# Kernel tuning notes

Hardware: AMD Instinct MI355X
Metric: run time of the kernel (lower is better)

The kernel has to match this reference:

```python
import jax, jax.numpy as jnp
import numpy as np

N_HEADS = 32
N_KV_HEADS = 8
HEAD_DIM = 64


def _apply_rope(x, cos, sin):
    # x: [b, s, h, d]; cos/sin: [s, d//2]; interleaved real/imag pairs
    xr = x[..., 0::2]
    xi = x[..., 1::2]
    c = cos[None, :, None, :]
    s = sin[None, :, None, :]
    out_r = xr * c - xi * s
    out_i = xr * s + xi * c
    return jnp.stack([out_r, out_i], axis=-1).reshape(x.shape)


def setup_inputs() -> dict:
    key = jax.random.key(0)
    ks = jax.random.split(key, 10)
    b, s, dim = 2, 512, 2048
    cache_len = 1536
    half = HEAD_DIM // 2
    pos = jnp.arange(cache_len, cache_len + s, dtype=jnp.float32)
    inv_freq = 1.0 / (10000.0 ** (jnp.arange(0, half, dtype=jnp.float32) / half))
    ang = pos[:, None] * inv_freq[None, :]
    scale = 0.02
    return {
        "x": jax.random.normal(ks[0], (b, s, dim), jnp.float32),
        "freqs_cos": jnp.cos(ang),
        "freqs_sin": jnp.sin(ang),
        "k_cache": jax.random.normal(ks[1], (b, N_KV_HEADS, cache_len, HEAD_DIM), jnp.float32),
        "v_cache": jax.random.normal(ks[2], (b, N_KV_HEADS, cache_len, HEAD_DIM), jnp.float32),
        "attn_mask": jnp.zeros((s, cache_len + s), jnp.float32),
        "wq": jax.random.normal(ks[3], (N_HEADS * HEAD_DIM, dim), jnp.float32) * scale,
        "wk": jax.random.normal(ks[4], (N_KV_HEADS * HEAD_DIM, dim), jnp.float32) * scale,
        "wv": jax.random.normal(ks[5], (N_KV_HEADS * HEAD_DIM, dim), jnp.float32) * scale,
        "wo": jax.random.normal(ks[6], (dim, N_HEADS * HEAD_DIM), jnp.float32) * scale,
    }


def reference(x, freqs_cos, freqs_sin, k_cache, v_cache, attn_mask, wq, wk, wv, wo):
    b, s, dim = x.shape
    n_rep = N_HEADS // N_KV_HEADS
    # QKV projections (nn.Linear: y = x @ W.T)
    q = (x @ wq.T).reshape(b, s, N_HEADS, HEAD_DIM)
    k = (x @ wk.T).reshape(b, s, N_KV_HEADS, HEAD_DIM)
    v = (x @ wv.T).reshape(b, s, N_KV_HEADS, HEAD_DIM)
    # RoPE on q, k
    q = _apply_rope(q, freqs_cos, freqs_sin)
    k = _apply_rope(k, freqs_cos, freqs_sin)
    # [b, h, s, d]
    q = q.transpose(0, 2, 1, 3)
    k = k.transpose(0, 2, 1, 3)
    v = v.transpose(0, 2, 1, 3)
    new_k, new_v = k, v
    # KV-cache concat along sequence dim
    k_full = jnp.concatenate([k_cache, k], axis=2)
    v_full = jnp.concatenate([v_cache, v], axis=2)
    # GQA: repeat_interleave kv heads
    if n_rep > 1:
        k_full = jnp.repeat(k_full, n_rep, axis=1)
        v_full = jnp.repeat(v_full, n_rep, axis=1)
    # SDPA
    scale = 1.0 / jnp.sqrt(jnp.asarray(HEAD_DIM, x.dtype))
    scores = jnp.einsum("bhqd,bhkd->bhqk", q, k_full) * scale + attn_mask
    probs = jax.nn.softmax(scores, axis=-1)
    out = jnp.einsum("bhqk,bhkd->bhqd", probs, v_full)
    out = out.transpose(0, 2, 1, 3).reshape(b, s, N_HEADS * HEAD_DIM)
    out = out @ wo.T
    return (out, new_k, new_v)
```

## Files before the change

kernel.cpp:

```cpp
#include <hip/hip_runtime.h>
#include <hip/hip_bf16.h>

typedef __attribute__((ext_vector_type(8))) short bf16x8;
typedef __attribute__((ext_vector_type(4))) float f32x4;
typedef unsigned short u16;

#define MFMA16(a, b, c) __builtin_amdgcn_mfma_f32_16x16x32_bf16(a, b, c, 0, 0, 0)
#define GLL(srcp, dstp) __builtin_amdgcn_global_load_lds(                      \
    (const __attribute__((address_space(1))) void*)(srcp),                     \
    (__attribute__((address_space(3))) void*)(dstp), 16, 0, 0)

__device__ __forceinline__ u16 f2b(float f) {
  union { float f; unsigned u; } a; a.f = f;
  return (u16)((a.u + 0x7FFFu + ((a.u >> 16) & 1u)) >> 16);
}
__device__ __forceinline__ unsigned pk2(float lo, float hi) {
  __hip_bfloat162 h = __float22bfloat162_rn(make_float2(lo, hi));
  return *reinterpret_cast<unsigned*>(&h);
}

__global__ __launch_bounds__(256) void prep(const float* __restrict__ x,
                                            const float* __restrict__ kc,
                                            u16* __restrict__ xb,
                                            u16* __restrict__ kfull) {
  const int c = blockIdx.x * 256 + threadIdx.x;
  const float* src;
  u16* dst;
  if (c < 524288) {
    src = x + (size_t)c * 4; dst = xb + (size_t)c * 4;
  } else {
    int l = c - 524288;
    int bh = l / 24576, r = l - bh * 24576;
    src = kc + (size_t)bh * 98304 + (size_t)r * 4;
    dst = kfull + (size_t)bh * 131072 + (size_t)r * 4;
  }
  const float4 v = *(const float4*)src;
  ushort4 o;
  o.x = f2b(v.x); o.y = f2b(v.y); o.z = f2b(v.z); o.w = f2b(v.w);
  *(ushort4*)dst = o;
}

__global__ __launch_bounds__(256) void vtr(const float* __restrict__ vc,
                                           const float* __restrict__ newv,
                                           u16* __restrict__ vT) {
  __shared__ float tile[64][65];
  const int kt = blockIdx.x, bh = blockIdx.y;
  const float* src;
  int colbase;
  if (kt < 24) {
    src = vc + ((size_t)bh * 1536 + (size_t)kt * 64) * 64;
    colbase = kt * 64;
  } else {
    src = newv + ((size_t)bh * 512 + (size_t)(kt - 24) * 64) * 64;
    colbase = 1536 + (kt - 24) * 64;
  }
  const int t = threadIdx.x;
#pragma unroll
  for (int j = 0; j < 4; j++) {
    int e = t + j * 256;
    int r = e >> 4, c = (e & 15) * 4;
    float4 v = *(const float4*)(src + (size_t)r * 64 + c);
    tile[r][c] = v.x; tile[r][c + 1] = v.y; tile[r][c + 2] = v.z; tile[r][c + 3] = v.w;
  }
  __syncthreads();
  int d = t >> 2, kv0 = (t & 3) * 16;
  u16* dst = vT + ((size_t)bh * 64 + d) * 2048 + colbase + (kv0 >> 4);
#pragma unroll
  for (int i = 0; i < 16; i++) dst[i * 4] = f2b(tile[kv0 + i][d]);
}

__global__ __launch_bounds__(256, 3) void gemm_bt(const u16* __restrict__ A,
                                                  const float* __restrict__ B0,
                                                  const float* __restrict__ B1,
                                                  const float* __restrict__ B2,
                                                  float* __restrict__ Cp,
                                                  int M, int N, int K, int nb1, int nb2) {
  __shared__ __attribute__((aligned(16))) u16 As[2][4096];
  __shared__ __attribute__((aligned(16))) u16 Bs[2][8192];
  const int t = threadIdx.x;
  const int lane = t & 63, w = t >> 6;
  const int wr = (w >> 1) * 32, wc = (w & 1) * 64;
  const int g = lane >> 4, cc = lane & 15;
  const int nby = N >> 7, cpx = nby >> 3, nrt = M >> 6;
  const int j = blockIdx.x & 7, q = blockIdx.x >> 3;
  const int ct = j * cpx + (q % cpx);
  const int rest = q / cpx;
  const int rt = rest % nrt, ks = rest / nrt;
  const size_t row0 = (size_t)rt * 64;
  const int col0 = ct * 128;
  const int k0base = ks * (K >> 1);

  const int lr = lane >> 3, lc = lane & 7;
  const int swz = lc ^ lr;
  const u16* aS = A + (row0 + w * 16 + lr) * (size_t)K + swz * 8 + k0base;
  const float* Bb;
  int brow;
  if (col0 < nb1) { Bb = B0; brow = col0; }
  else if (col0 < nb2) { Bb = B1; brow = col0 - nb1; }
  else { Bb = B2; brow = col0 - nb2; }
  const float* bS = Bb + (brow + w * 32 + lr) * (size_t)K + swz * 8 + k0base;

  f32x4 acc[2][4] = {};
  f32x4 blA[4][2], blB[4][2];

#define ALOAD(bufi, kk0)                                                       \
  {                                                                            \
    _Pragma("unroll") for (int i = 0; i < 2; i++)                              \
        GLL(aS + (size_t)(i * 8) * K + (kk0), &As[bufi][(w * 16 + i * 8) * 64]); \
  }
#define BLOAD(blv, kk0)                                                        \
  {                                                                            \
    _Pragma("unroll") for (int i = 0; i < 4; i++) {                            \
      blv[i][0] = *(const f32x4*)(bS + (size_t)(i * 8) * K + (kk0));           \
      blv[i][1] = *(const f32x4*)(bS + (size_t)(i * 8) * K + (kk0) + 4);       \
    }                                                                          \
  }
#define BWRITE(blv, bufi)                                                      \
  {                                                                            \
    _Pragma("unroll") for (int i = 0; i < 4; i++) {                            \
      uint4 pw;                                                                \
      pw.x = pk2(blv[i][0][0], blv[i][0][1]);                                  \
      pw.y = pk2(blv[i][0][2], blv[i][0][3]);                                  \
      pw.z = pk2(blv[i][1][0], blv[i][1][1]);                                  \
      pw.w = pk2(blv[i][1][2], blv[i][1][3]);                                  \
      *(uint4*)&Bs[bufi][(w * 32 + i * 8 + lr) * 64 + lc * 8] = pw;            \
    }                                                                          \
  }

  const int niter = (K >> 1) >> 6;

  ALOAD(0, 0);
  BLOAD(blA, 0);
  BWRITE(blA, 0);
  BLOAD(blB, 64);
  asm volatile("s_waitcnt lgkmcnt(0)" ::: "memory");
  __builtin_amdgcn_s_barrier();

#define GBODY(it_, blPrev, blCur)                                              \
  {                                                                            \
    const int buf = (it_) & 1;                                                 \
    if ((it_) > 0) {                                                           \
      if ((it_) + 1 < niter) {                                                 \
        asm volatile("s_waitcnt vmcnt(8)" ::: "memory");                       \
      } else {                                                                 \
        asm volatile("s_waitcnt vmcnt(0)" ::: "memory");                       \
      }                                                                        \
      asm volatile("s_waitcnt lgkmcnt(0)" ::: "memory");                       \
      __builtin_amdgcn_s_barrier();                                            \
    }                                                                          \
    if ((it_) + 1 < niter) ALOAD(buf ^ 1, ((it_) + 1) * 64);                   \
    if ((it_) + 2 < niter) BLOAD(blCur, ((it_) + 2) * 64);                     \
    bf16x8 av[2][2], bv[4][2];                                                 \
    _Pragma("unroll") for (int m = 0; m < 2; m++) {                            \
      const int row = wr + m * 16 + cc;                                        \
      _Pragma("unroll") for (int kk = 0; kk < 2; kk++)                         \
          av[m][kk] =                                                          \
              *(const bf16x8*)(&As[buf][row * 64 + (((kk * 4 + g) ^ (cc & 7)) * 8)]); \
    }                                                                          \
    _Pragma("unroll") for (int n = 0; n < 4; n++) {                            \
      const int row = wc + n * 16 + cc;                                        \
      _Pragma("unroll") for (int kk = 0; kk < 2; kk++)                         \
          bv[n][kk] =                                                          \
              *(const bf16x8*)(&Bs[buf][row * 64 + (((kk * 4 + g) ^ (cc & 7)) * 8)]); \
    }                                                                          \
    _Pragma("unroll") for (int kk = 0; kk < 2; kk++)                           \
        _Pragma("unroll") for (int m = 0; m < 2; m++)                          \
        _Pragma("unroll") for (int n = 0; n < 4; n++)                          \
            acc[m][n] = MFMA16(av[m][kk], bv[n][kk], acc[m][n]);               \
    if ((it_) + 1 < niter) BWRITE(blPrev, buf ^ 1);                            \
  }

  for (int it = 0; it < niter; it += 2) {
    GBODY(it, blB, blA);
    GBODY(it + 1, blA, blB);
  }
#undef GBODY
#undef ALOAD
#undef BLOAD
#undef BWRITE

  float* Cw = Cp + (size_t)ks * M * N;
#pragma unroll
  for (int m = 0; m < 2; m++)
#pragma unroll
    for (int n = 0; n < 4; n++)
#pragma unroll
      for (int r = 0; r < 4; r++)
        Cw[(row0 + wr + m * 16 + g * 4 + r) * N + (col0 + wc + n * 16 + cc)] = acc[m][n][r];
}

__global__ __launch_bounds__(256) void postproc(const float* __restrict__ Cp0,
                                                const float* __restrict__ Cp1,
                                                const float* __restrict__ fcos,
                                                const float* __restrict__ fsin,
                                                u16* __restrict__ qrope,
                                                u16* __restrict__ kfull,
                                                float* __restrict__ newk,
                                                float* __restrict__ newv) {
  int idx = blockIdx.x * 256 + threadIdx.x;
  if (idx >= 1024 * 1536) return;
  int m = idx / 1536, p = idx - m * 1536;
  int b = m >> 9, s = m & 511;
  const float* r0 = Cp0 + (size_t)m * 3072;
  const float* r1 = Cp1 + (size_t)m * 3072;
  if (p < 1280) {
    bool isq = p < 1024;
    int pk = isq ? p : p - 1024;
    int h = pk >> 5, i = pk & 31;
    int colbase = (isq ? 0 : 2048) + h * 64 + 2 * i;
    float xr = r0[colbase] + r1[colbase];
    float xi = r0[colbase + 1] + r1[colbase + 1];
    float co = fcos[s * 32 + i], si = fsin[s * 32 + i];
    float orr = xr * co - xi * si;
    float oii = xr * si + xi * co;
    if (isq) {
      u16* dst = qrope + (((size_t)(b * 32 + h) * 512 + s) * 64 + 2 * i);
      dst[0] = f2b(orr); dst[1] = f2b(oii);
    } else {
      size_t o0 = ((size_t)(b * 8 + h) * 512 + s) * 64 + 2 * i;
      newk[o0] = orr; newk[o0 + 1] = oii;
      u16* kf = kfull + (((size_t)(b * 8 + h) * 2048 + 1536 + s) * 64 + 2 * i);
      kf[0] = f2b(orr); kf[1] = f2b(oii);
    }
  } else {
    int pv = p - 1280;
    int h = pv >> 5, i = pv & 31;
    int cb = 2560 + h * 64 + 2 * i;
    float v0 = r0[cb] + r1[cb], v1 = r0[cb + 1] + r1[cb + 1];
    size_t o0 = ((size_t)(b * 8 + h) * 512 + s) * 64 + 2 * i;
    newv[o0] = v0; newv[o0 + 1] = v1;
  }
}

__global__ __launch_bounds__(256) void sumout(const float* __restrict__ a,
                                              const float* __restrict__ b,
                                              float* __restrict__ out) {
  const int i = blockIdx.x * 256 + threadIdx.x;
  const float4 va = *(const float4*)(a + (size_t)i * 4);
  const float4 vb = *(const float4*)(b + (size_t)i * 4);
  float4 o;
  o.x = va.x + vb.x; o.y = va.y + vb.y; o.z = va.z + vb.z; o.w = va.w + vb.w;
  *(float4*)(out + (size_t)i * 4) = o;
}

__global__ __launch_bounds__(512, 4) void attn_split(const u16* __restrict__ qrope,
                                                     const u16* __restrict__ kfull,
                                                     const u16* __restrict__ vT,
                                                     const float* __restrict__ mask,
                                                     float* __restrict__ po,
                                                     float* __restrict__ ml) {
  __shared__ __attribute__((aligned(16))) u16 Ks[4][4096];
  __shared__ __attribute__((aligned(16))) u16 Vs[4][4096];
  __shared__ __attribute__((aligned(16))) u16 P_lds[8192];
  const int t = threadIdx.x, lane = t & 63, w = t >> 6;
  const int g = lane >> 4, cc = lane & 15;
  const int p = blockIdx.x;
  const int v = (p & 7) * 64 + (p >> 3);
  const int bh = v >> 3, qt = (v >> 1) & 3, sp = v & 1;
  const int b = bh >> 5, h = bh & 31;
  const int bhkv = b * 8 + (h >> 2);
  const int s0 = qt * 128 + w * 16;
  const int j0beg = sp * 1024;

  const int lr = lane >> 3, lc = lane & 7;
  const int swzc = lc ^ lr;

  bf16x8 qa0, qa1;
  {
    const u16* qb = qrope + ((size_t)bh * 512 + s0 + cc) * 64 + g * 8;
    qa0 = *(const bf16x8*)qb;
    qa1 = *(const bf16x8*)(qb + 32);
  }
  float mrow[4], lsum[4];
  f32x4 o[4] = {};
#pragma unroll
  for (int r = 0; r < 4; r++) { mrow[r] = -1e30f; lsum[r] = 0.0f; }

  u16* Pw = P_lds + w * 1024;
  const float* mbase = mask + (size_t)(s0 + g * 4) * 2048 + cc;
  const u16* ksrc0 = kfull + (size_t)bhkv * 131072 + (size_t)(w * 8 + lr) * 64 + swzc * 8;
  const u16* vsrc0 = vT + ((size_t)bhkv * 64 + w * 8 + lr) * 2048 + swzc * 8;

#pragma unroll
  for (int pt = 0; pt < 3; ++pt) {
    GLL(ksrc0 + (size_t)(j0beg + pt * 64) * 64, &Ks[pt][w * 512]);
    GLL(vsrc0 + (j0beg + pt * 64), &Vs[pt][w * 512]);
  }

  for (int it = 0; it < 16; ++it) {
    const int buf = it & 3;
    const int j0 = j0beg + it * 64;
    if (it < 14) {
      asm volatile("s_waitcnt vmcnt(4)" ::: "memory");
    } else if (it == 14) {
      asm volatile("s_waitcnt vmcnt(2)" ::: "memory");
    } else {
      asm volatile("s_waitcnt vmcnt(0)" ::: "memory");
    }
    __builtin_amdgcn_s_barrier();

    float mk[4][4];
#pragma unroll
    for (int r = 0; r < 4; r++)
#pragma unroll
      for (int jb = 0; jb < 4; jb++)
        mk[r][jb] = mbase[(size_t)r * 2048 + j0 + jb * 16];
    __builtin_amdgcn_sched_barrier(0);
    if (it < 13) {
      GLL(ksrc0 + (size_t)(j0 + 192) * 64, &Ks[(it + 3) & 3][w * 512]);
      GLL(vsrc0 + (j0 + 192), &Vs[(it + 3) & 3][w * 512]);
    }

    f32x4 sc[4];
    __builtin_amdgcn_s_setprio(1);
#pragma unroll
    for (int jb = 0; jb < 4; jb++) {
      const bf16x8 k0 = *(const bf16x8*)(&Ks[buf][(jb * 16 + cc) * 64 + ((g ^ (cc & 7)) * 8)]);
      const bf16x8 k1 =
          *(const bf16x8*)(&Ks[buf][(jb * 16 + cc) * 64 + (((g + 4) ^ (cc & 7)) * 8)]);
      f32x4 z = {0.f, 0.f, 0.f, 0.f};
      z = MFMA16(qa0, k0, z);
      z = MFMA16(qa1, k1, z);
      sc[jb] = z;
    }
    __builtin_amdgcn_s_setprio(0);
    float pp[4][4];
#pragma unroll
    for (int r = 0; r < 4; r++) {
#pragma unroll
      for (int jb = 0; jb < 4; jb++)
        pp[r][jb] = sc[jb][r] * 0.125f + mk[r][jb];
      const float lm = fmaxf(fmaxf(pp[r][0], pp[r][1]), fmaxf(pp[r][2], pp[r][3]));
      if (__any(lm > mrow[r] + 8.0f)) {
        float tm = lm;
#pragma unroll
        for (int off = 1; off < 16; off <<= 1) tm = fmaxf(tm, __shfl_xor(tm, off, 64));
        const float newm = fmaxf(mrow[r], tm);
        const float corr = __expf(mrow[r] - newm);
        mrow[r] = newm;
        lsum[r] *= corr;
#pragma unroll
        for (int db = 0; db < 4; db++) o[db][r] *= corr;
      }
      float ps = 0.f;
#pragma unroll
      for (int jb = 0; jb < 4; jb++) { pp[r][jb] = __expf(pp[r][jb] - mrow[r]); ps += pp[r][jb]; }
      lsum[r] += ps;
      const int rowb = (g * 4 + r) * 128;
      const int sw = ((g * 4 + r) & 7) << 4;
      uint2 pw;
      pw.x = pk2(pp[r][0], pp[r][1]);
      pw.y = pk2(pp[r][2], pp[r][3]);
      *(uint2*)((char*)Pw + ((rowb + cc * 8) ^ sw)) = pw;
    }
    __builtin_amdgcn_s_setprio(1);
#pragma unroll
    for (int kk = 0; kk < 2; kk++) {
      const bf16x8 pa =
          *(const bf16x8*)(Pw + (((cc * 128 + kk * 64 + g * 16) ^ ((cc & 7) << 4)) >> 1));
#pragma unroll
      for (int db = 0; db < 4; db++) {
        const bf16x8 vf =
            *(const bf16x8*)(&Vs[buf][(db * 16 + cc) * 64 + (((kk * 4 + g) ^ (cc & 7)) * 8)]);
        o[db] = MFMA16(pa, vf, o[db]);
      }
    }
    __builtin_amdgcn_s_setprio(0);
  }
#pragma unroll
  for (int r = 0; r < 4; r++) {
    float ps = lsum[r];
#pragma unroll
    for (int off = 1; off < 16; off <<= 1) ps += __shfl_xor(ps, off, 64);
    const size_t row = (size_t)bh * 512 + s0 + g * 4 + r;
    float* dst = po + (row * 2 + sp) * 64 + cc;
#pragma unroll
    for (int db = 0; db < 4; db++) dst[db * 16] = o[db][r];
    if (cc == 0) {
      float2* mlp = (float2*)ml;
      mlp[row * 2 + sp] = make_float2(mrow[r], ps);
    }
  }
}

__global__ __launch_bounds__(256) void attn_combine(const float* __restrict__ po,
                                                    const float* __restrict__ ml,
                                                    u16* __restrict__ aout) {
  const int t = threadIdx.x;
  const int row = blockIdx.x * 4 + (t >> 6);
  const int d = t & 63;
  const int bh = row >> 9, s = row & 511;
  const int b = bh >> 5, h = bh & 31;
  const float2* mlp = (const float2*)ml;
  const float2 m0 = mlp[row * 2 + 0], m1 = mlp[row * 2 + 1];
  const float M = fmaxf(m0.x, m1.x);
  const float w0 = __expf(m0.x - M), w1 = __expf(m1.x - M);
  const float L = m0.y * w0 + m1.y * w1;
  const float o = po[(size_t)(row * 2 + 0) * 64 + d] * w0 +
                  po[(size_t)(row * 2 + 1) * 64 + d] * w1;
  aout[((size_t)(b * 512 + s)) * 2048 + h * 64 + d] = f2b(o / L);
}

extern "C" void kernel_launch(void* const* d_in, const int* in_sizes, int n_in,
                              void* d_out, int out_size, void* d_ws, size_t ws_size,
                              hipStream_t stream) {
  (void)in_sizes; (void)n_in; (void)out_size; (void)ws_size;
  const float* x    = (const float*)d_in[0];
  const float* fcos = (const float*)d_in[1];
  const float* fsin = (const float*)d_in[2];
  const float* kc   = (const float*)d_in[3];
  const float* vc   = (const float*)d_in[4];
  const float* mask = (const float*)d_in[5];
  const float* wq   = (const float*)d_in[6];
  const float* wk   = (const float*)d_in[7];
  const float* wv   = (const float*)d_in[8];
  const float* wo   = (const float*)d_in[9];

  float* out_f = (float*)d_out;
  float* newk  = out_f + 2097152;
  float* newv  = out_f + 2621440;

  u16*   xb    = (u16*)d_ws;
  float* Cp    = (float*)(xb + 2097152);
  float* Cp1   = Cp + 3145728;
  u16*   qrope = (u16*)(Cp + 6291456);
  u16*   kfull = qrope + 2097152;
  u16*   vTf   = kfull + 2097152;
  u16*   aout  = vTf + 2097152;
  float* ml    = (float*)(aout + 2097152);
  float* po    = (float*)d_ws;
  float* Co    = (float*)d_ws;
  float* Co1   = Co + 2097152;

  prep<<<3584, 256, 0, stream>>>(x, kc, xb, kfull);

  gemm_bt<<<768, 256, 0, stream>>>(xb, wq, wk, wv, Cp,
                                   1024, 3072, 2048, 2048, 2560);
  postproc<<<6144, 256, 0, stream>>>(Cp, Cp1, fcos, fsin, qrope, kfull, newk, newv);
  vtr<<<dim3(32, 16), 256, 0, stream>>>(vc, newv, vTf);
  attn_split<<<512, 512, 0, stream>>>(qrope, kfull, vTf, mask, po, ml);
  attn_combine<<<8192, 256, 0, stream>>>(po, ml, aout);
  gemm_bt<<<512, 256, 0, stream>>>(aout, wo, wo, wo, Co,
                                   1024, 2048, 2048, 4096, 8192);
  sumout<<<2048, 256, 0, stream>>>(Co, Co1, out_f);
}
```

Measured before the change: 121.2 us.

## Split each attention block into two interleaved KV streams with independent softmax state

Each wave now runs two independent online-softmax accumulators over two halves of its KV range, which cuts the loop from 16 to 8 iterations, each handling two 64-key tiles. The QK MFMAs for the second stream are issued while the first stream's softmax and PV run, aiming to hide exp/shuffle latency behind matrix work. Prefetch changes from a 3-deep ring to double buffering with a full vmcnt(0) wait, which may expose more load latency. It also raises register pressure and adds a merge of the two partial results at the end.

```diff
diff --git a/kernel.cpp b/kernel.cpp
--- a/kernel.cpp
+++ b/kernel.cpp
@@ -271,89 +271,99 @@
     qa0 = *(const bf16x8*)qb;
     qa1 = *(const bf16x8*)(qb + 32);
   }
-  float mrow[4], lsum[4];
-  f32x4 o[4] = {};
-#pragma unroll
-  for (int r = 0; r < 4; r++) { mrow[r] = -1e30f; lsum[r] = 0.0f; }
+  float m0[4], l0[4], m1[4], l1[4];
+  f32x4 oa[4] = {}, ob[4] = {};
+#pragma unroll
+  for (int r = 0; r < 4; r++) { m0[r] = -1e30f; l0[r] = 0.f; m1[r] = -1e30f; l1[r] = 0.f; }
 
   u16* Pw = P_lds + w * 1024;
   const float* mbase = mask + (size_t)(s0 + g * 4) * 2048 + cc;
   const u16* ksrc0 = kfull + (size_t)bhkv * 131072 + (size_t)(w * 8 + lr) * 64 + swzc * 8;
   const u16* vsrc0 = vT + ((size_t)bhkv * 64 + w * 8 + lr) * 2048 + swzc * 8;
-
-#pragma unroll
-  for (int pt = 0; pt < 3; ++pt) {
-    GLL(ksrc0 + (size_t)(j0beg + pt * 64) * 64, &Ks[pt][w * 512]);
-    GLL(vsrc0 + (j0beg + pt * 64), &Vs[pt][w * 512]);
-  }
-
-  for (int it = 0; it < 16; ++it) {
-    const int buf = it & 3;
+  const u16* ksrc1 = ksrc0 + 512 * 64;
+  const u16* vsrc1 = vsrc0 + 512;
+
+  GLL(ksrc0 + (size_t)j0beg * 64, &Ks[0][w * 512]);
+  GLL(vsrc0 + j0beg, &Vs[0][w * 512]);
+  GLL(ksrc1 + (size_t)j0beg * 64, &Ks[2][w * 512]);
+  GLL(vsrc1 + j0beg, &Vs[2][w * 512]);
+
+  for (int it = 0; it < 8; ++it) {
+    const int bu = it & 1;
     const int j0 = j0beg + it * 64;
-    if (it < 14) {
-      asm volatile("s_waitcnt vmcnt(4)" ::: "memory");
-    } else if (it == 14) {
-      asm volatile("s_waitcnt vmcnt(2)" ::: "memory");
-    } else {
-      asm volatile("s_waitcnt vmcnt(0)" ::: "memory");
-    }
+    asm volatile("s_waitcnt vmcnt(0)" ::: "memory");
     __builtin_amdgcn_s_barrier();
 
-    float mk[4][4];
+    float mk0[4][4], mk1[4][4];
 #pragma unroll
     for (int r = 0; r < 4; r++)
 #pragma unroll
-      for (int jb = 0; jb < 4; jb++)
-        mk[r][jb] = mbase[(size_t)r * 2048 + j0 + jb * 16];
+      for (int jb = 0; jb < 4; jb++) {
+        mk0[r][jb] = mbase[(size_t)r * 2048 + j0 + jb * 16];
+        mk1[r][jb] = mbase[(size_t)r * 2048 + j0 + 512 + jb * 16];
+      }
     __builtin_amdgcn_sched_barrier(0);
-    if (it < 13) {
-      GLL(ksrc0 + (size_t)(j0 + 192) * 64, &Ks[(it + 3) & 3][w * 512]);
-      GLL(vsrc0 + (j0 + 192), &Vs[(it + 3) & 3][w * 512]);
-    }
-
-    f32x4 sc[4];
+    if (it < 7) {
+      GLL(ksrc0 + (size_t)(j0 + 64) * 64, &Ks[bu ^ 1][w * 512]);
+      GLL(vsrc0 + (j0 + 64), &Vs[bu ^ 1][w * 512]);
+      GLL(ksrc1 + (size_t)(j0 + 64) * 64, &Ks[2 + (bu ^ 1)][w * 512]);
+      GLL(vsrc1 + (j0 + 64), &Vs[2 + (bu ^ 1)][w * 512]);
+    }
+
+    f32x4 sc0[4];
     __builtin_amdgcn_s_setprio(1);
 #pragma unroll
     for (int jb = 0; jb < 4; jb++) {
-      const bf16x8 k0 = *(const bf16x8*)(&Ks[buf][(jb * 16 + cc) * 64 + ((g ^ (cc & 7)) * 8)]);
+      const bf16x8 k0 = *(const bf16x8*)(&Ks[bu][(jb * 16 + cc) * 64 + ((g ^ (cc & 7)) * 8)]);
       const bf16x8 k1 =
-          *(const bf16x8*)(&Ks[buf][(jb * 16 + cc) * 64 + (((g + 4) ^ (cc & 7)) * 8)]);
+          *(const bf16x8*)(&Ks[bu][(jb * 16 + cc) * 64 + (((g + 4) ^ (cc & 7)) * 8)]);
       f32x4 z = {0.f, 0.f, 0.f, 0.f};
       z = MFMA16(qa0, k0, z);
       z = MFMA16(qa1, k1, z);
-      sc[jb] = z;
+      sc0[jb] = z;
     }
     __builtin_amdgcn_s_setprio(0);
-    float pp[4][4];
 #pragma unroll
     for (int r = 0; r < 4; r++) {
-#pragma unroll
-      for (int jb = 0; jb < 4; jb++)
-        pp[r][jb] = sc[jb][r] * 0.125f + mk[r][jb];
-      const float lm = fmaxf(fmaxf(pp[r][0], pp[r][1]), fmaxf(pp[r][2], pp[r][3]));
-      if (__any(lm > mrow[r] + 8.0f)) {
+      float pp[4];
+#pragma unroll
+      for (int jb = 0; jb < 4; jb++) pp[jb] = sc0[jb][r] * 0.125f + mk0[r][jb];
+      const float lm = fmaxf(fmaxf(pp[0], pp[1]), fmaxf(pp[2], pp[3]));
+      if (__any(lm > m0[r] + 8.0f)) {
         float tm = lm;
 #pragma unroll
         for (int off = 1; off < 16; off <<= 1) tm = fmaxf(tm, __shfl_xor(tm, off, 64));
-        const float newm = fmaxf(mrow[r], tm);
-        const float corr = __expf(mrow[r] - newm);
-        mrow[r] = newm;
-        lsum[r] *= corr;
-#pragma unroll
-        for (int db = 0; db < 4; db++) o[db][r] *= corr;
+        const float newm = fmaxf(m0[r], tm);
+        const float corr = __expf(m0[r] - newm);
+        m0[r] = newm;
+        l0[r] *= corr;
+#pragma unroll
+        for (int db = 0; db < 4; db++) oa[db][r] *= corr;
       }
       float ps = 0.f;
 #pragma unroll
-      for (int jb = 0; jb < 4; jb++) { pp[r][jb] = __expf(pp[r][jb] - mrow[r]); ps += pp[r][jb]; }
-      lsum[r] += ps;
+      for (int jb = 0; jb < 4; jb++) { pp[jb] = __expf(pp[jb] - m0[r]); ps += pp[jb]; }
+      l0[r] += ps;
       const int rowb = (g * 4 + r) * 128;
       const int sw = ((g * 4 + r) & 7) << 4;
       uint2 pw;
-      pw.x = pk2(pp[r][0], pp[r][1]);
-      pw.y = pk2(pp[r][2], pp[r][3]);
+      pw.x = pk2(pp[0], pp[1]);
+      pw.y = pk2(pp[2], pp[3]);
       *(uint2*)((char*)Pw + ((rowb + cc * 8) ^ sw)) = pw;
     }
+    f32x4 sc1[4];
     __builtin_amdgcn_s_setprio(1);
+#pragma unroll
+    for (int jb = 0; jb < 4; jb++) {
+      const bf16x8 k0 =
+          *(const bf16x8*)(&Ks[2 + bu][(jb * 16 + cc) * 64 + ((g ^ (cc & 7)) * 8)]);
+      const bf16x8 k1 =
+          *(const bf16x8*)(&Ks[2 + bu][(jb * 16 + cc) * 64 + (((g + 4) ^ (cc & 7)) * 8)]);
+      f32x4 z = {0.f, 0.f, 0.f, 0.f};
+      z = MFMA16(qa0, k0, z);
+      z = MFMA16(qa1, k1, z);
+      sc1[jb] = z;
+    }
 #pragma unroll
     for (int kk = 0; kk < 2; kk++) {
       const bf16x8 pa =
@@ -361,24 +371,67 @@
 #pragma unroll
       for (int db = 0; db < 4; db++) {
         const bf16x8 vf =
-            *(const bf16x8*)(&Vs[buf][(db * 16 + cc) * 64 + (((kk * 4 + g) ^ (cc & 7)) * 8)]);
-        o[db] = MFMA16(pa, vf, o[db]);
+            *(const bf16x8*)(&Vs[bu][(db * 16 + cc) * 64 + (((kk * 4 + g) ^ (cc & 7)) * 8)]);
+        oa[db] = MFMA16(pa, vf, oa[db]);
       }
     }
     __builtin_amdgcn_s_setprio(0);
+#pragma unroll
+    for (int r = 0; r < 4; r++) {
+      float pp[4];
+#pragma unroll
+      for (int jb = 0; jb < 4; jb++) pp[jb] = sc1[jb][r] * 0.125f + mk1[r][jb];
+      const float lm = fmaxf(fmaxf(pp[0], pp[1]), fmaxf(pp[2], pp[3]));
+      if (__any(lm > m1[r] + 8.0f)) {
+        float tm = lm;
+#pragma unroll
+        for (int off = 1; off < 16; off <<= 1) tm = fmaxf(tm, __shfl_xor(tm, off, 64));
+        const float newm = fmaxf(m1[r], tm);
+        const float corr = __expf(m1[r] - newm);
+        m1[r] = newm;
+        l1[r] *= corr;
+#pragma unroll
+        for (int db = 0; db < 4; db++) ob[db][r] *= corr;
+      }
+      float ps = 0.f;
+#pragma unroll
+      for (int jb = 0; jb < 4; jb++) { pp[jb] = __expf(pp[jb] - m1[r]); ps += pp[jb]; }
+      l1[r] += ps;
+      const int rowb = (g * 4 + r) * 128;
+      const int sw = ((g * 4 + r) & 7) << 4;
+      uint2 pw;
+      pw.x = pk2(pp[0], pp[1]);
+      pw.y = pk2(pp[2], pp[3]);
+      *(uint2*)((char*)Pw + ((rowb + cc * 8) ^ sw)) = pw;
+    }
+    __builtin_amdgcn_s_setprio(1);
+#pragma unroll
+    for (int kk = 0; kk < 2; kk++) {
+      const bf16x8 pa =
+          *(const bf16x8*)(Pw + (((cc * 128 + kk * 64 + g * 16) ^ ((cc & 7) << 4)) >> 1));
+#pragma unroll
+      for (int db = 0; db < 4; db++) {
+        const bf16x8 vf =
+            *(const bf16x8*)(&Vs[2 + bu][(db * 16 + cc) * 64 + (((kk * 4 + g) ^ (cc & 7)) * 8)]);
+        ob[db] = MFMA16(pa, vf, ob[db]);
+      }
+    }
+    __builtin_amdgcn_s_setprio(0);
   }
 #pragma unroll
   for (int r = 0; r < 4; r++) {
-    float ps = lsum[r];
+    const float M = fmaxf(m0[r], m1[r]);
+    const float w0 = __expf(m0[r] - M), w1 = __expf(m1[r] - M);
+    float ps = l0[r] * w0 + l1[r] * w1;
 #pragma unroll
     for (int off = 1; off < 16; off <<= 1) ps += __shfl_xor(ps, off, 64);
     const size_t row = (size_t)bh * 512 + s0 + g * 4 + r;
     float* dst = po + (row * 2 + sp) * 64 + cc;
 #pragma unroll
-    for (int db = 0; db < 4; db++) dst[db * 16] = o[db][r];
+    for (int db = 0; db < 4; db++) dst[db * 16] = oa[db][r] * w0 + ob[db][r] * w1;
     if (cc == 0) {
       float2* mlp = (float2*)ml;
-      mlp[row * 2 + sp] = make_float2(mrow[r], ps);
+      mlp[row * 2 + sp] = make_float2(M, ps);
     }
   }
 }
```

Measured after the change: 167.7 us. 1.38x slower.
